# Kernel tuning notes

Measured on AMD Instinct MI355X. Metric: run time of the kernel, lower is better.

Reference implementation:

```python
import jax, jax.numpy as jnp
import numpy as np

NEG_SLOPE = 0.2


def setup_inputs() -> dict:
    key = jax.random.key(0)
    k1, k2, k3, k4, k5 = jax.random.split(key, 5)
    N, E = 50000, 800000
    IN, H, O = 128, 4, 32
    x = jax.random.normal(k1, (N, IN), dtype=jnp.float32)
    edge_index = jax.random.randint(k2, (2, E), 0, N, dtype=jnp.int64)
    weight = jax.random.normal(k3, (IN, H, O), dtype=jnp.float32) * 0.05
    att_weight = jax.random.normal(k4, (H, 2 * O), dtype=jnp.float32) * 0.05
    bias = jax.random.normal(k5, (H * O,), dtype=jnp.float32) * 0.05
    return {"x": x, "edge_index": edge_index, "weight": weight,
            "att_weight": att_weight, "bias": bias}


def reference(x, edge_index, weight, att_weight, bias):
    # GAT forward, eval mode (dropout=0), concat=True.
    N = x.shape[0]
    H, O = weight.shape[1], weight.shape[2]
    # Linear transform: [N, H, O]
    h = jnp.einsum('ni,iho->nho', x, weight)
    src, dst = edge_index[0], edge_index[1]  # message src -> dst
    h_i = h[dst]   # target features per edge  [E, H, O]
    h_j = h[src]   # source features per edge  [E, H, O]
    # Attention logits: leaky_relu(att . [h_i || h_j])  -> [E, H]
    a_i, a_j = att_weight[:, :O], att_weight[:, O:]
    alpha = jnp.einsum('eho,ho->eh', h_i, a_i) + jnp.einsum('eho,ho->eh', h_j, a_j)
    alpha = jax.nn.leaky_relu(alpha, NEG_SLOPE)
    # Segment softmax over incoming edges of each dst node.
    amax = jax.ops.segment_max(alpha, dst, num_segments=N)      # [N, H]
    ex = jnp.exp(alpha - amax[dst])                             # [E, H]
    denom = jax.ops.segment_sum(ex, dst, num_segments=N)        # [N, H]
    coef = ex / (denom[dst] + 1e-16)                            # [E, H]
    # Weighted scatter-aggregate of source messages.
    out = jax.ops.segment_sum(h_j * coef[..., None], dst, num_segments=N)  # [N, H, O]
    out = out.reshape(N, H * O) + bias
    return out
```

## Files before the change

### kernel.cpp

```cpp
#include <hip/hip_runtime.h>
#include <hip/hip_fp16.h>
#include <math.h>

#define NEG_SLOPE 0.2f

typedef __attribute__((ext_vector_type(8))) short bf16x8;
typedef __attribute__((ext_vector_type(4))) short short4v;
typedef __attribute__((ext_vector_type(4))) float f32x4;
typedef __attribute__((ext_vector_type(8))) unsigned short u16x8;

__device__ __forceinline__ float lrelu(float x) { return x > 0.f ? x : NEG_SLOPE * x; }

__device__ __forceinline__ short f2bf(float f) {
    unsigned u = __float_as_uint(f);
    u += 0x7fff + ((u >> 16) & 1);
    return (short)(u >> 16);
}

__global__ __launch_bounds__(256) void k_gemm(const float* __restrict__ x,
                                              const float* __restrict__ w,
                                              const float* __restrict__ att,
                                              __half* __restrict__ hout,
                                              float* __restrict__ adi,
                                              float* __restrict__ adj,
                                              int* __restrict__ gcur, int N) {
    __shared__ short SH[24576];
    const int t = threadIdx.x;
    const int row0 = blockIdx.x * 64;

    if (blockIdx.x == 0) {
        gcur[t] = 0; gcur[t + 256] = 0; gcur[t + 512] = 0; gcur[t + 768] = 0;
    }

    #pragma unroll
    for (int i = 0; i < 8; ++i) {
        int idx = t + 256 * i;
        int r = idx >> 5, c4 = (idx & 31) * 4;
        float4 v = make_float4(0.f, 0.f, 0.f, 0.f);
        if (row0 + r < N) v = *(const float4*)(x + (size_t)(row0 + r) * 128 + c4);
        short4v sv;
        sv.x = f2bf(v.x); sv.y = f2bf(v.y); sv.z = f2bf(v.z); sv.w = f2bf(v.w);
        *(short4v*)&SH[(r * 128 + c4) ^ ((r & 7) << 3)] = sv;
    }
    {
        int c = t & 127, kh = (t >> 7) * 64;
        for (int kb = 0; kb < 16; ++kb) {
            int k = kh + kb * 4;
            short4v sv;
            sv.x = f2bf(w[(size_t)(k + 0) * 128 + c]);
            sv.y = f2bf(w[(size_t)(k + 1) * 128 + c]);
            sv.z = f2bf(w[(size_t)(k + 2) * 128 + c]);
            sv.w = f2bf(w[(size_t)(k + 3) * 128 + c]);
            *(short4v*)&SH[8192 + ((c * 128 + k) ^ ((c & 7) << 3))] = sv;
        }
    }
    __syncthreads();

    const int wv = t >> 6, lane = t & 63;
    const int lr = lane & 15, kg = lane >> 4;

    f32x4 acc[8];
    #pragma unroll
    for (int n = 0; n < 8; ++n) acc[n] = (f32x4){0.f, 0.f, 0.f, 0.f};

    #pragma unroll
    for (int kk = 0; kk < 4; ++kk) {
        const int k0 = kk * 32 + kg * 8;
        int r = wv * 16 + lr;
        bf16x8 a = *(const bf16x8*)&SH[(r * 128 + k0) ^ ((r & 7) << 3)];
        bf16x8 b[8];
        #pragma unroll
        for (int n = 0; n < 8; ++n) {
            int c = n * 16 + lr;
            b[n] = *(const bf16x8*)&SH[8192 + ((c * 128 + k0) ^ ((c & 7) << 3))];
        }
        #pragma unroll
        for (int n = 0; n < 8; ++n)
            acc[n] = __builtin_amdgcn_mfma_f32_16x16x32_bf16(a, b[n], acc[n], 0, 0, 0);
    }

    #pragma unroll
    for (int reg = 0; reg < 4; ++reg) {
        int r = row0 + wv * 16 + kg * 4 + reg;
        if (r < N) {
            __half* hp = hout + (size_t)r * 128 + lr;
            #pragma unroll
            for (int n = 0; n < 8; ++n)
                hp[n * 16] = __float2half(acc[n][reg]);
        }
    }

    __syncthreads();
    float* attF = (float*)&SH[8192];
    attF[t] = att[t];
    #pragma unroll
    for (int reg = 0; reg < 4; ++reg) {
        int row = wv * 16 + kg * 4 + reg;
        #pragma unroll
        for (int n = 0; n < 8; ++n) {
            int col = n * 16 + lr;
            SH[(row * 128 + col) ^ ((row & 7) << 3)] =
                (short)__half_as_ushort(__float2half(acc[n][reg]));
        }
    }
    __syncthreads();
    {
        int row = t >> 2, head = t & 3;
        int grow = row0 + row;
        if (grow < N) {
            float si = 0.f, sj = 0.f;
            #pragma unroll
            for (int j = 0; j < 32; ++j) {
                int jj = (j + row) & 31;
                float hv = __half2float(__ushort_as_half(
                    (unsigned short)SH[(row * 128 + head * 32 + jj) ^ ((row & 7) << 3)]));
                si += hv * attF[head * 64 + jj];
                sj += hv * attF[head * 64 + 32 + jj];
            }
            adi[grow * 4 + head] = si;
            adj[grow * 4 + head] = sj;
        }
    }
}

__global__ __launch_bounds__(512) void k_bin(const int* __restrict__ ei,
                                             int* __restrict__ gcur,
                                             unsigned* __restrict__ bins,
                                             int E, int nbkt, int cap) {
    __shared__ int lcnt[1024];
    __shared__ int lbase[1024];
    const int t = threadIdx.x;
    lcnt[t] = 0; lcnt[t + 512] = 0;
    __syncthreads();

    const int e0 = blockIdx.x * 4096;
    const int ne = min(4096, E - e0);

    int bkt[8], rank[8];
    unsigned pk[8];
    #pragma unroll
    for (int k = 0; k < 8; ++k) {
        int idx = t + k * 512;
        if (idx < ne) {
            int e = e0 + idx;
            int src = ei[e], dst = ei[E + e];
            int b = dst >> 6;
            bkt[k] = b;
            pk[k] = ((unsigned)(dst & 63) << 24) | (unsigned)src;
            rank[k] = atomicAdd(&lcnt[b], 1);
        } else bkt[k] = -1;
    }
    __syncthreads();
    for (int j = t; j < nbkt; j += 512)
        if (lcnt[j] > 0) lbase[j] = atomicAdd(&gcur[j], lcnt[j]);
    __syncthreads();
    #pragma unroll
    for (int k = 0; k < 8; ++k) {
        if (bkt[k] >= 0)
            bins[(size_t)bkt[k] * cap + lbase[bkt[k]] + rank[k]] = pk[k];
    }
}

__global__ __launch_bounds__(256) void k_bucket(const unsigned* __restrict__ bins,
                                                const int* __restrict__ gcur,
                                                int* __restrict__ begG,
                                                int* __restrict__ degG,
                                                int* __restrict__ csr,
                                                int N, int cap) {
    __shared__ int cnt[64];
    __shared__ int beg[64];
    __shared__ int cur[64];
    const int b = blockIdx.x, t = threadIdx.x;
    const int sz = min(gcur[b], cap);
    const unsigned* myb = bins + (size_t)b * cap;
    int* mycsr = csr + (size_t)b * cap;

    if (t < 64) cnt[t] = 0;
    __syncthreads();
    for (int i = t; i < sz; i += 256) atomicAdd(&cnt[myb[i] >> 24], 1);
    __syncthreads();
    if (t < 64) {
        int v = cnt[t];
        int s = v;
        #pragma unroll
        for (int off = 1; off < 64; off <<= 1) {
            int u = __shfl_up(s, off);
            if (t >= off) s += u;
        }
        beg[t] = s - v;
        cur[t] = s - v;
        int node = b * 64 + t;
        if (node < N) { begG[node] = b * cap + (s - v); degG[node] = v; }
    }
    __syncthreads();
    for (int i = t; i < sz; i += 256) {
        unsigned p = myb[i];
        int pos = atomicAdd(&cur[p >> 24], 1);
        mycsr[pos] = (int)(p & 0xFFFFFFu);
    }
}

__global__ __launch_bounds__(256) void k_node(const int* __restrict__ begG,
                                              const int* __restrict__ degG,
                                              const int* __restrict__ csr,
                                              const __half* __restrict__ h,
                                              const float* __restrict__ adi,
                                              const float* __restrict__ adjf,
                                              const float* __restrict__ bias,
                                              float* __restrict__ out, int N) {
    int node = (blockIdx.x * blockDim.x + threadIdx.x) >> 6;
    if (node >= N) return;
    const int lane = threadIdx.x & 63;
    const int q = lane >> 4, s = lane & 15;
    const int head = s >> 2;

    const int beg = begG[node];
    const int deg = degG[node];
    const float ai = adi[node * 4 + head];

    float acc[8] = {0.f, 0.f, 0.f, 0.f, 0.f, 0.f, 0.f, 0.f};
    float dsum = 0.f;

    for (int i = 0; i < deg; i += 16) {
        int idx[4];
        float aj[4];
        u16x8 hv[4];
        #pragma unroll
        for (int bb = 0; bb < 4; ++bb) {
            int ee = i + 4 * bb + q;
            idx[bb] = csr[beg + (ee < deg ? ee : 0)];
        }
        #pragma unroll
        for (int bb = 0; bb < 4; ++bb) {
            aj[bb] = adjf[idx[bb] * 4 + head];
            hv[bb] = *(const u16x8*)(h + (size_t)idx[bb] * 128 + s * 8);
        }
        #pragma unroll
        for (int bb = 0; bb < 4; ++bb) {
            int ee = i + 4 * bb + q;
            float ex = (ee < deg) ? __expf(lrelu(ai + aj[bb])) : 0.f;
            dsum += ex;
            #pragma unroll
            for (int k = 0; k < 8; ++k)
                acc[k] += __half2float(__ushort_as_half(hv[bb][k])) * ex;
        }
    }

    #pragma unroll
    for (int k = 0; k < 8; ++k) {
        acc[k] += __shfl_xor(acc[k], 16);
        acc[k] += __shfl_xor(acc[k], 32);
    }
    dsum += __shfl_xor(dsum, 16);
    dsum += __shfl_xor(dsum, 32);

    if (q == 0) {
        float inv = 1.f / (dsum + 1e-16f);
        const float4* b4 = (const float4*)(bias + s * 8);
        float4 bv0 = b4[0], bv1 = b4[1];
        float4 o0 = make_float4(acc[0] * inv + bv0.x, acc[1] * inv + bv0.y,
                                acc[2] * inv + bv0.z, acc[3] * inv + bv0.w);
        float4 o1 = make_float4(acc[4] * inv + bv1.x, acc[5] * inv + bv1.y,
                                acc[6] * inv + bv1.z, acc[7] * inv + bv1.w);
        float4* op = (float4*)(out + (size_t)node * 128 + s * 8);
        op[0] = o0;
        op[1] = o1;
    }
}

extern "C" void kernel_launch(void* const* d_in, const int* in_sizes, int n_in,
                              void* d_out, int out_size, void* d_ws, size_t ws_size,
                              hipStream_t stream) {
    const float* x    = (const float*)d_in[0];
    const int*   ei   = (const int*)d_in[1];
    const float* w    = (const float*)d_in[2];
    const float* att  = (const float*)d_in[3];
    const float* bias = (const float*)d_in[4];

    const int N = in_sizes[0] / 128;
    const int E = in_sizes[1] / 2;

    const int NBKT = (N + 63) >> 6;
    const int CAP  = 1536;

    float* out = (float*)d_out;
    char*  wsb = (char*)d_ws;

    __half* h   = (__half*)wsb;
    float*  adi = (float*)(wsb + (size_t)N * 128 * 2);
    float*  adj = adi + (size_t)N * 4;
    int* gcur   = (int*)(adj + (size_t)N * 4);
    int* begG   = gcur + 1024;
    int* degG   = begG + N;
    int* csr    = degG + N;
    unsigned* bins = (unsigned*)(csr + (size_t)NBKT * CAP);

    k_gemm<<<(N + 63) / 64, 256, 0, stream>>>(x, w, att, h, adi, adj, gcur, N);
    k_bin<<<(E + 4095) / 4096, 512, 0, stream>>>(ei, gcur, bins, E, NBKT, CAP);
    k_bucket<<<NBKT, 256, 0, stream>>>(bins, gcur, begG, degG, csr, N, CAP);

    {
        long long total = (long long)N * 64;
        int blocks = (int)((total + 255) / 256);
        k_node<<<blocks, 256, 0, stream>>>(begG, degG, csr, (const __half*)h,
                                           adi, adj, bias, out, N);
    }
}
```

Before: 76.25 us.

## Store node features head-major and process one head per wavefront in aggregation

The GEMM now writes h and the attention scalars in head-major planes ([H][N][32] and [H][N]). The aggregation kernel maps each wavefront to one (node, head) pair with 16 edges per pass, so each gathered row is 64 bytes of one head rather than 256 bytes. Block ids interleave heads so blocks running at the same time touch one head plane at a time, which is meant to improve cache locality of the random gathers. The cost is four times as many wavefronts, each re-reading the CSR index list and doing a longer shuffle reduction.

```diff
diff --git a/kernel.cpp b/kernel.cpp
--- a/kernel.cpp
+++ b/kernel.cpp
@@ -20,9 +20,9 @@
 __global__ __launch_bounds__(256) void k_gemm(const float* __restrict__ x,
                                               const float* __restrict__ w,
                                               const float* __restrict__ att,
-                                              __half* __restrict__ hout,
-                                              float* __restrict__ adi,
-                                              float* __restrict__ adj,
+                                              __half* __restrict__ hH,
+                                              float* __restrict__ aiH,
+                                              float* __restrict__ ajH,
                                               int* __restrict__ gcur, int N) {
     __shared__ short SH[24576];
     const int t = threadIdx.x;
@@ -83,10 +83,10 @@
     for (int reg = 0; reg < 4; ++reg) {
         int r = row0 + wv * 16 + kg * 4 + reg;
         if (r < N) {
-            __half* hp = hout + (size_t)r * 128 + lr;
             #pragma unroll
             for (int n = 0; n < 8; ++n)
-                hp[n * 16] = __float2half(acc[n][reg]);
+                hH[(size_t)(n >> 1) * N * 32 + (size_t)r * 32 + (n & 1) * 16 + lr] =
+                    __float2half(acc[n][reg]);
         }
     }
 
@@ -117,8 +117,8 @@
                 si += hv * attF[head * 64 + jj];
                 sj += hv * attF[head * 64 + 32 + jj];
             }
-            adi[grow * 4 + head] = si;
-            adj[grow * 4 + head] = sj;
+            aiH[(size_t)head * N + grow] = si;
+            ajH[(size_t)head * N + grow] = sj;
         }
     }
 }
@@ -168,7 +168,6 @@
                                                 int* __restrict__ csr,
                                                 int N, int cap) {
     __shared__ int cnt[64];
-    __shared__ int beg[64];
     __shared__ int cur[64];
     const int b = blockIdx.x, t = threadIdx.x;
     const int sz = min(gcur[b], cap);
@@ -187,7 +186,6 @@
             int u = __shfl_up(s, off);
             if (t >= off) s += u;
         }
-        beg[t] = s - v;
         cur[t] = s - v;
         int node = b * 64 + t;
         if (node < N) { begG[node] = b * cap + (s - v); degG[node] = v; }
@@ -203,66 +201,68 @@
 __global__ __launch_bounds__(256) void k_node(const int* __restrict__ begG,
                                               const int* __restrict__ degG,
                                               const int* __restrict__ csr,
-                                              const __half* __restrict__ h,
-                                              const float* __restrict__ adi,
-                                              const float* __restrict__ adjf,
+                                              const __half* __restrict__ hH,
+                                              const float* __restrict__ aiH,
+                                              const float* __restrict__ ajH,
                                               const float* __restrict__ bias,
                                               float* __restrict__ out, int N) {
-    int node = (blockIdx.x * blockDim.x + threadIdx.x) >> 6;
+    const int bid = blockIdx.x;
+    const int slot = bid & 7, g = bid >> 3;
+    const int head = slot >> 1;
+    const int nb = g * 2 + (slot & 1);
+    const int wv = threadIdx.x >> 6;
+    const int node = nb * 4 + wv;
     if (node >= N) return;
     const int lane = threadIdx.x & 63;
-    const int q = lane >> 4, s = lane & 15;
-    const int head = s >> 2;
+    const int e = lane >> 2, s = lane & 3;
 
     const int beg = begG[node];
     const int deg = degG[node];
-    const float ai = adi[node * 4 + head];
+    const float ai = aiH[(size_t)head * N + node];
+    const __half* hb = hH + (size_t)head * N * 32 + s * 8;
+    const float* ajb = ajH + (size_t)head * N;
 
     float acc[8] = {0.f, 0.f, 0.f, 0.f, 0.f, 0.f, 0.f, 0.f};
     float dsum = 0.f;
 
-    for (int i = 0; i < deg; i += 16) {
-        int idx[4];
-        float aj[4];
-        u16x8 hv[4];
-        #pragma unroll
-        for (int bb = 0; bb < 4; ++bb) {
-            int ee = i + 4 * bb + q;
-            idx[bb] = csr[beg + (ee < deg ? ee : 0)];
-        }
-        #pragma unroll
-        for (int bb = 0; bb < 4; ++bb) {
-            aj[bb] = adjf[idx[bb] * 4 + head];
-            hv[bb] = *(const u16x8*)(h + (size_t)idx[bb] * 128 + s * 8);
-        }
-        #pragma unroll
-        for (int bb = 0; bb < 4; ++bb) {
-            int ee = i + 4 * bb + q;
-            float ex = (ee < deg) ? __expf(lrelu(ai + aj[bb])) : 0.f;
-            dsum += ex;
-            #pragma unroll
-            for (int k = 0; k < 8; ++k)
-                acc[k] += __half2float(__ushort_as_half(hv[bb][k])) * ex;
-        }
+    for (int i = 0; i < deg; i += 32) {
+        int e0 = i + e, e1 = i + 16 + e;
+        int i0 = csr[beg + (e0 < deg ? e0 : 0)];
+        int i1 = csr[beg + (e1 < deg ? e1 : 0)];
+        float aj0 = ajb[i0];
+        float aj1 = ajb[i1];
+        u16x8 h0 = *(const u16x8*)(hb + (size_t)i0 * 32);
+        u16x8 h1 = *(const u16x8*)(hb + (size_t)i1 * 32);
+        float ex0 = (e0 < deg) ? __expf(lrelu(ai + aj0)) : 0.f;
+        float ex1 = (e1 < deg) ? __expf(lrelu(ai + aj1)) : 0.f;
+        dsum += ex0 + ex1;
+        #pragma unroll
+        for (int k = 0; k < 8; ++k)
+            acc[k] += __half2float(__ushort_as_half(h0[k])) * ex0
+                    + __half2float(__ushort_as_half(h1[k])) * ex1;
     }
 
     #pragma unroll
     for (int k = 0; k < 8; ++k) {
+        acc[k] += __shfl_xor(acc[k], 4);
+        acc[k] += __shfl_xor(acc[k], 8);
         acc[k] += __shfl_xor(acc[k], 16);
         acc[k] += __shfl_xor(acc[k], 32);
     }
+    dsum += __shfl_xor(dsum, 4);
+    dsum += __shfl_xor(dsum, 8);
     dsum += __shfl_xor(dsum, 16);
     dsum += __shfl_xor(dsum, 32);
 
-    if (q == 0) {
+    if (e == 0) {
         float inv = 1.f / (dsum + 1e-16f);
-        const float4* b4 = (const float4*)(bias + s * 8);
+        const float4* b4 = (const float4*)(bias + head * 32 + s * 8);
         float4 bv0 = b4[0], bv1 = b4[1];
         float4 o0 = make_float4(acc[0] * inv + bv0.x, acc[1] * inv + bv0.y,
                                 acc[2] * inv + bv0.z, acc[3] * inv + bv0.w);
         float4 o1 = make_float4(acc[4] * inv + bv1.x, acc[5] * inv + bv1.y,
                                 acc[6] * inv + bv1.z, acc[7] * inv + bv1.w);
-        float4* op = (float4*)(out + (size_t)node * 128 + s * 8);
+        float4* op = (float4*)(out + (size_t)node * 128 + head * 32 + s * 8);
         op[0] = o0;
         op[1] = o1;
     }
@@ -286,23 +286,23 @@
     float* out = (float*)d_out;
     char*  wsb = (char*)d_ws;
 
-    __half* h   = (__half*)wsb;
-    float*  adi = (float*)(wsb + (size_t)N * 128 * 2);
-    float*  adj = adi + (size_t)N * 4;
-    int* gcur   = (int*)(adj + (size_t)N * 4);
+    __half* hH  = (__half*)wsb;
+    float*  aiH = (float*)(wsb + (size_t)N * 128 * 2);
+    float*  ajH = aiH + (size_t)N * 4;
+    int* gcur   = (int*)(ajH + (size_t)N * 4);
     int* begG   = gcur + 1024;
     int* degG   = begG + N;
     int* csr    = degG + N;
     unsigned* bins = (unsigned*)(csr + (size_t)NBKT * CAP);
 
-    k_gemm<<<(N + 63) / 64, 256, 0, stream>>>(x, w, att, h, adi, adj, gcur, N);
+    k_gemm<<<(N + 63) / 64, 256, 0, stream>>>(x, w, att, hH, aiH, ajH, gcur, N);
     k_bin<<<(E + 4095) / 4096, 512, 0, stream>>>(ei, gcur, bins, E, NBKT, CAP);
     k_bucket<<<NBKT, 256, 0, stream>>>(bins, gcur, begG, degG, csr, N, CAP);
 
     {
-        long long total = (long long)N * 64;
-        int blocks = (int)((total + 255) / 256);
-        k_node<<<blocks, 256, 0, stream>>>(begG, degG, csr, (const __half*)h,
-                                           adi, adj, bias, out, N);
-    }
-}
+        const int nquads = (N + 3) / 4;
+        const int groups = (nquads + 1) / 2;
+        k_node<<<groups * 8, 256, 0, stream>>>(begG, degG, csr, (const __half*)hH,
+                                               aiH, ajH, bias, out, N);
+    }
+}
```

Measured after the change: 118.6 us. 55.5% more time.
